# Kernel optimization log

Measured on AMD Instinct MI355X. Metric: run time of the kernel, lower is better.

The kernel has to match this reference:

```python
import jax, jax.numpy as jnp
import numpy as np

B, S, D = 64, 512, 768
CLAUSE = 5  # words per clause


def _ragged():
    w = 64 + (np.arange(B) * 37) % 57              # words per sentence, max 120
    mw = int(w.max())
    Wt = int(w.sum())                               # 5899 total words
    word2sent = np.repeat(np.arange(B), w)
    word_pos = np.concatenate([np.arange(n) for n in w])
    t = 1 + (np.arange(Wt) * 13) % 4                # tokens per word
    word_seg = np.repeat(np.arange(Wt), t)          # token -> word id
    tok_sent = word2sent[word_seg]                  # sorted by sentence
    tok_pos = np.concatenate([np.arange(c) for c in np.bincount(tok_sent, minlength=B)])
    token_indices = tok_sent * S + tok_pos          # clause tokens are the first tokens of each row
    clause_seg = np.arange(Wt) // CLAUSE
    n_clauses = (Wt + CLAUSE - 1) // CLAUSE
    return w, mw, word2sent, word_pos, word_seg, token_indices, clause_seg, n_clauses


def setup_inputs() -> dict:
    key = jax.random.key(0)
    ks = jax.random.split(key, 12)
    w, mw, word2sent, word_pos, word_seg, token_indices, clause_seg, n_clauses = _ragged()
    sequence_output = jax.random.normal(ks[0], (B, S, D), dtype=jnp.float32)
    # sparse-ish adjacency, zeroed beyond each sentence's real word count
    adj = (jax.random.uniform(ks[1], (B, mw, mw)) < 0.1).astype(jnp.float32)
    valid = (jnp.arange(mw)[None, :] < jnp.asarray(w)[:, None]).astype(jnp.float32)
    adj = adj * valid[:, :, None] * valid[:, None, :]
    stdv = 1.0 / np.sqrt(D)
    u = lambda k, shp, s: jax.random.uniform(k, shp, minval=-s, maxval=s, dtype=jnp.float32)
    inp = {
        'sequence_output': sequence_output,
        'adj': adj,
        'W1': u(ks[2], (D, D), stdv), 'b1': u(ks[3], (D,), stdv),
        'W2': u(ks[4], (D, D), stdv), 'b2': u(ks[5], (D,), stdv),
        'W3': u(ks[6], (D, D), stdv), 'b3': u(ks[7], (D,), stdv),
        'Wfc': u(ks[8], (D, 16), stdv), 'bfc': u(ks[9], (16,), stdv),
        'token_indices': jnp.asarray(token_indices, jnp.int32),
        'word_seg': jnp.asarray(word_seg, jnp.int32),
        'word2sent': jnp.asarray(word2sent, jnp.int32),
        'word_pos': jnp.asarray(word_pos, jnp.int32),
        'clause_seg': jnp.asarray(clause_seg, jnp.int32),
        'n_clauses': int(n_clauses),
    }
    return inp


def reference(sequence_output, adj, W1, b1, W2, b2, W3, b3, Wfc, bfc,
              token_indices, word_seg, word2sent, word_pos, clause_seg, n_clauses):
    d = sequence_output.shape[-1]
    Wt = word2sent.shape[0]
    mw = adj.shape[1]
    # masked_select of clause tokens -> [N_tok, D]
    tokens = sequence_output.reshape(-1, d)[token_indices]
    # per-word max over its tokens (torch.split + stack(max))
    word_out = jax.ops.segment_max(tokens, word_seg, num_segments=Wt)
    # pad words into [B, max_words, D] (original pads with randn; adj zeroes pad nodes)
    x = jnp.zeros((adj.shape[0], mw, d), word_out.dtype).at[word2sent, word_pos].set(word_out)
    denom = jnp.sum(adj, axis=2, keepdims=True) + 1.0
    def gcn(h, W, b):
        return jnp.einsum('bij,bjd->bid', adj, h @ W) / denom + b
    x = jax.nn.relu(gcn(x, W1, b1))
    x = jax.nn.relu(gcn(x, W2, b2))
    x = jax.nn.relu(gcn(x, W3, b3))
    # unpad back to ragged word list, then per-clause max
    words_back = x[word2sent, word_pos]
    clause_out = jax.ops.segment_max(words_back, clause_seg, num_segments=n_clauses)
    logits = clause_out @ Wfc + bfc
    return logits
```

## Files before the change

### kernel.cpp

```cpp
#include <hip/hip_runtime.h>
#include <hip/hip_bf16.h>
#include <cfloat>

#define BB   64
#define SS   512
#define DD   768
#define MW   120
#define MPAD 6016
#define TS8  12288
#define WT   5899
#define NC   1180

typedef __attribute__((ext_vector_type(4))) int intx4;

#define SXS  (6.5032f/16255.0f)
#define ISX  (16255.0f/6.5032f)
#define SWS  (0.03610243f/16255.0f)
#define ISW  (16255.0f/0.03610243f)
#define DQ1  (SXS*SWS*16384.0f)
#define DQ2  (SXS*SWS*128.0f)

#define AS3(p) ((__attribute__((address_space(3))) void*)(p))
#define AS1(p) ((const __attribute__((address_space(1))) void*)(p))

__device__ __forceinline__ int swz8(int r, int k) {
    return (r >> 4) * TS8 + (k >> 4) * 256 + (r & 15) * 16 + (k & 15);
}

__device__ __forceinline__ void q8(float x, float inv_s, char& h, char& l) {
    float q = x * inv_s;
    float qh = rintf(q * 0.0078125f);
    qh = fminf(fmaxf(qh, -127.f), 127.f);
    float ql = rintf(fmaf(-128.f, qh, q));
    ql = fminf(fmaxf(ql, -127.f), 127.f);
    h = (char)(int)qh; l = (char)(int)ql;
}

__device__ __forceinline__ int wstart_cf(int w) {
    const int pp[4] = {0, 0, 1, 3};
    return w + 6 * (w >> 2) + pp[w & 3];
}
__device__ __forceinline__ int sent_words(int b) { return 64 + (b * 37) % 57; }

#define NBL_NBR 2560
#define NBL_QW  2304

__global__ __launch_bounds__(192) void setup_k(
    const float* __restrict__ adj,
    const float* __restrict__ W1, const float* __restrict__ W2, const float* __restrict__ W3,
    const float* __restrict__ seq, const int* __restrict__ tok_idx,
    char* __restrict__ qWh, char* __restrict__ qWl,
    char* __restrict__ Qah, char* __restrict__ Qal,
    int* __restrict__ nbr, int* __restrict__ cnt, float* __restrict__ rdenom,
    int* __restrict__ sstart) {
    const int blk = blockIdx.x;
    const int tid = threadIdx.x;
    if (blk < NBL_NBR) {
        int row = blk * 3 + (tid >> 6);
        int lane = tid & 63;
        const float* r = adj + (size_t)row * MW;
        float v0 = r[lane];
        float v1 = (lane + 64 < MW) ? r[lane + 64] : 0.0f;
        unsigned long long m0 = __ballot(v0 != 0.0f);
        unsigned long long m1 = __ballot(v1 != 0.0f);
        unsigned long long below = (1ull << lane) - 1ull;
        int c0 = __popcll(m0);
        int* nb = nbr + (size_t)row * MW;
        if (v0 != 0.0f) nb[__popcll(m0 & below)] = lane;
        if (v1 != 0.0f) nb[c0 + __popcll(m1 & below)] = lane + 64;
        if (lane == 0) {
            int c = c0 + __popcll(m1);
            cnt[row] = c;
            rdenom[row] = 1.0f / (float)(c + 1);
        }
    } else if (blk < NBL_NBR + NBL_QW) {
        int idx = (blk - NBL_NBR) * 192 + tid;
        int l = idx / (DD * DD / 4);
        int rem = idx - l * (DD * DD / 4);
        int kg = rem / DD, n = rem - kg * DD;
        int k = kg * 4;
        const float* W = (l == 0) ? W1 : (l == 1) ? W2 : W3;
        char h[4], lo[4];
        #pragma unroll
        for (int u = 0; u < 4; ++u)
            q8(W[(size_t)(k + u) * DD + n], ISW, h[u], lo[u]);
        int off = l * (DD * DD) + swz8(n, k);
        *(char4*)(qWh + off) = make_char4(h[0], h[1], h[2], h[3]);
        *(char4*)(qWl + off) = make_char4(lo[0], lo[1], lo[2], lo[3]);
    } else if (blk < NBL_NBR + NBL_QW + WT) {
        int w = blk - (NBL_NBR + NBL_QW);
        int t = tid;
        int s = wstart_cf(w), e = wstart_cf(w + 1);
        float4 acc = make_float4(-FLT_MAX, -FLT_MAX, -FLT_MAX, -FLT_MAX);
        for (int i = s; i < e; ++i) {
            int row = tok_idx[i];
            float4 v = *(const float4*)(seq + (size_t)row * DD + t * 4);
            acc.x = fmaxf(acc.x, v.x); acc.y = fmaxf(acc.y, v.y);
            acc.z = fmaxf(acc.z, v.z); acc.w = fmaxf(acc.w, v.w);
        }
        char h[4], lo[4];
        q8(acc.x, ISX, h[0], lo[0]); q8(acc.y, ISX, h[1], lo[1]);
        q8(acc.z, ISX, h[2], lo[2]); q8(acc.w, ISX, h[3], lo[3]);
        int off = swz8(w, t * 4);
        *(char4*)(Qah + off) = make_char4(h[0], h[1], h[2], h[3]);
        *(char4*)(Qal + off) = make_char4(lo[0], lo[1], lo[2], lo[3]);
    } else {
        if (tid == 0) {
            int acc = 0;
            for (int b = 0; b < BB; ++b) { sstart[b] = acc; acc += sent_words(b); }
            sstart[BB] = acc;
        }
    }
}


__global__ __launch_bounds__(256) void gemm8_k(const char* __restrict__ Qah,
                                               const char* __restrict__ Qal,
                                               const char* __restrict__ Qbh,
                                               const char* __restrict__ Qbl,
                                               float* __restrict__ H) {
    __shared__ char lds[49152];
    const int g = blockIdx.x;
    const int xcd = g & 7;
    const int q2 = g >> 3;
    const int nt = q2 % 12;
    const int mt = xcd * 12 + q2 / 12;
    if (mt >= 94) return;

    const int tid = threadIdx.x;
    const int lane = tid & 63;
    const int wave = tid >> 6;
    const int wm = wave >> 1, wn = wave & 1;
    const int bm4 = mt * 4, bn4 = nt * 4;

    const int to = lane * 16;
    const char* gAh = Qah + (size_t)(bm4 + wave) * TS8 + to;
    const char* gAl = Qal + (size_t)(bm4 + wave) * TS8 + to;
    const char* gBh = Qbh + (size_t)(bn4 + wave) * TS8 + to;
    const char* gBl = Qbl + (size_t)(bn4 + wave) * TS8 + to;
    char* ldst = &lds[wave * 1024 + to];

    auto stage = [&](int kt, int buf) {
        const int bo = buf * 16384;
        const int ko = kt * 1024;
        __builtin_amdgcn_global_load_lds(AS1(gAh + ko), AS3(ldst + bo),         16, 0, 0);
        __builtin_amdgcn_global_load_lds(AS1(gAl + ko), AS3(ldst + bo + 4096),  16, 0, 0);
        __builtin_amdgcn_global_load_lds(AS1(gBh + ko), AS3(ldst + bo + 8192),  16, 0, 0);
        __builtin_amdgcn_global_load_lds(AS1(gBl + ko), AS3(ldst + bo + 12288), 16, 0, 0);
    };

    intx4 acc1[2][2] = {}, acc2[2][2] = {};

    stage(0, 0);
    stage(1, 1);
    #pragma unroll
    for (int kt = 0; kt < 12; ++kt) {
        const int buf = kt % 3;
        if (kt < 11) { asm volatile("s_waitcnt vmcnt(4)" ::: "memory"); }
        else         { asm volatile("s_waitcnt vmcnt(0)" ::: "memory"); }
        __builtin_amdgcn_s_barrier();
        asm volatile("" ::: "memory");
        if (kt < 10) stage(kt + 2, (kt + 2) % 3);

        const char* lb = &lds[buf * 16384];
        intx4 ah[2], al[2], bh[2], bl[2];
        #pragma unroll
        for (int i = 0; i < 2; ++i) {
            ah[i] = *(const intx4*)(lb + (wm * 2 + i) * 1024 + lane * 16);
            al[i] = *(const intx4*)(lb + 4096 + (wm * 2 + i) * 1024 + lane * 16);
        }
        #pragma unroll
        for (int j = 0; j < 2; ++j) {
            bh[j] = *(const intx4*)(lb + 8192 + (wn * 2 + j) * 1024 + lane * 16);
            bl[j] = *(const intx4*)(lb + 12288 + (wn * 2 + j) * 1024 + lane * 16);
        }
        #pragma unroll
        for (int i = 0; i < 2; ++i)
            #pragma unroll
            for (int j = 0; j < 2; ++j) {
                acc1[i][j] = __builtin_amdgcn_mfma_i32_16x16x64_i8(ah[i], bh[j], acc1[i][j], 0, 0, 0);
                acc2[i][j] = __builtin_amdgcn_mfma_i32_16x16x64_i8(ah[i], bl[j], acc2[i][j], 0, 0, 0);
                acc2[i][j] = __builtin_amdgcn_mfma_i32_16x16x64_i8(al[i], bh[j], acc2[i][j], 0, 0, 0);
            }
    }

    const int q = lane >> 4, c = lane & 15;
    #pragma unroll
    for (int i = 0; i < 2; ++i) {
        #pragma unroll
        for (int r = 0; r < 4; ++r) {
            int row = mt * 64 + (wm * 2 + i) * 16 + q * 4 + r;
            float* out = H + (size_t)row * DD + nt * 64 + wn * 32 + c;
            #pragma unroll
            for (int j = 0; j < 2; ++j)
                out[j * 16] = (float)acc1[i][j][r] * DQ1 + (float)acc2[i][j][r] * DQ2;
        }
    }
}

__global__ void combine_k(const float* __restrict__ H, const int* __restrict__ w2s,
                          const int* __restrict__ sstart, const int* __restrict__ nbr,
                          const int* __restrict__ cnt, const float* __restrict__ rdenom,
                          const float* __restrict__ bias,
                          char* __restrict__ Qah, char* __restrict__ Qal,
                          float* __restrict__ Xf, int writef32) {
    int g = blockIdx.x;
    int w = (g & 7) * 768 + (g >> 3);
    if (w >= WT) return;
    int t = threadIdx.x;
    int s = w2s[w];
    int w0 = sstart[s];
    int bi = s * MW + (w - w0);
    int n = cnt[bi];
    float rd = rdenom[bi];
    const int* nb = nbr + (size_t)bi * MW;
    float4 acc = make_float4(0.f, 0.f, 0.f, 0.f);
    for (int k = 0; k < n; ++k) {
        int row = w0 + nb[k];
        float4 v = *(const float4*)(H + (size_t)row * DD + t * 4);
        acc.x += v.x; acc.y += v.y; acc.z += v.z; acc.w += v.w;
    }
    float4 bv = *(const float4*)(bias + t * 4);
    float4 o;
    o.x = fmaxf(fmaf(acc.x, rd, bv.x), 0.f);
    o.y = fmaxf(fmaf(acc.y, rd, bv.y), 0.f);
    o.z = fmaxf(fmaf(acc.z, rd, bv.z), 0.f);
    o.w = fmaxf(fmaf(acc.w, rd, bv.w), 0.f);
    if (writef32) {
        *(float4*)(Xf + (size_t)w * DD + t * 4) = o;
    } else {
        char h[4], lo[4];
        q8(o.x, ISX, h[0], lo[0]); q8(o.y, ISX, h[1], lo[1]);
        q8(o.z, ISX, h[2], lo[2]); q8(o.w, ISX, h[3], lo[3]);
        int off = swz8(w, t * 4);
        *(char4*)(Qah + off) = make_char4(h[0], h[1], h[2], h[3]);
        *(char4*)(Qal + off) = make_char4(lo[0], lo[1], lo[2], lo[3]);
    }
}

__global__ __launch_bounds__(192) void clause_k(const float* __restrict__ Xf,
                                                const float* __restrict__ Wfc,
                                                const float* __restrict__ bfc,
                                                float* __restrict__ out) {
    __shared__ float cm[DD];
    __shared__ float part[12][16];
    int c = blockIdx.x;
    int t = threadIdx.x;
    int s = c * 5, e = min(c * 5 + 5, WT);
    float4 m = make_float4(-FLT_MAX, -FLT_MAX, -FLT_MAX, -FLT_MAX);
    for (int w = s; w < e; ++w) {
        float4 v = *(const float4*)(Xf + (size_t)w * DD + t * 4);
        m.x = fmaxf(m.x, v.x); m.y = fmaxf(m.y, v.y);
        m.z = fmaxf(m.z, v.z); m.w = fmaxf(m.w, v.w);
    }
    *(float4*)&cm[t * 4] = m;
    __syncthreads();
    int o = t & 15, gg = t >> 4;
    float p = 0.f;
    #pragma unroll 4
    for (int d = gg * 64; d < gg * 64 + 64; ++d)
        p = fmaf(cm[d], Wfc[d * 16 + o], p);
    part[gg][o] = p;
    __syncthreads();
    if (t < 16) {
        float acc = bfc[t];
        #pragma unroll
        for (int g2 = 0; g2 < 12; ++g2) acc += part[g2][t];
        out[c * 16 + t] = acc;
    }
}

extern "C" void kernel_launch(void* const* d_in, const int* in_sizes, int n_in,
                              void* d_out, int out_size, void* d_ws, size_t ws_size,
                              hipStream_t stream) {
    const float* seq  = (const float*)d_in[0];
    const float* adj  = (const float*)d_in[1];
    const float* W1   = (const float*)d_in[2];
    const float* b1   = (const float*)d_in[3];
    const float* W2   = (const float*)d_in[4];
    const float* b2   = (const float*)d_in[5];
    const float* W3   = (const float*)d_in[6];
    const float* b3   = (const float*)d_in[7];
    const float* Wfc  = (const float*)d_in[8];
    const float* bfc  = (const float*)d_in[9];
    const int* tok_idx = (const int*)d_in[10];
    const int* w2s     = (const int*)d_in[12];

    char* p = (char*)d_ws;
    char* Qah = p; p += (size_t)MPAD * DD;
    char* Qal = p; p += (size_t)MPAD * DD;
    float* H  = (float*)p; p += (size_t)MPAD * DD * 4;
    char* qWh = p; p += (size_t)3 * DD * DD;
    char* qWl = p; p += (size_t)3 * DD * DD;
    float* Xf = (float*)p; p += (size_t)MPAD * DD * 4;
    int* nbr    = (int*)p;    p += (size_t)BB * MW * MW * 4;
    int* cnt    = (int*)p;    p += (size_t)BB * MW * 4;
    float* rde  = (float*)p;  p += (size_t)BB * MW * 4;
    int* sstart = (int*)p;    p += (size_t)(BB + 1) * 4;

    setup_k<<<NBL_NBR + NBL_QW + WT + 1, 192, 0, stream>>>(
        adj, W1, W2, W3, seq, tok_idx, qWh, qWl, Qah, Qal, nbr, cnt, rde, sstart);

    const float* bs[3] = {b1, b2, b3};
    for (int l = 0; l < 3; ++l) {
        gemm8_k<<<1152, 256, 0, stream>>>(
            Qah, Qal, qWh + (size_t)l * DD * DD, qWl + (size_t)l * DD * DD, H);
        combine_k<<<8 * 768, 192, 0, stream>>>(H, w2s, sstart, nbr, cnt, rde, bs[l],
                                               Qah, Qal, Xf, l == 2 ? 1 : 0);
    }

    clause_k<<<NC, 192, 0, stream>>>(Xf, Wfc, bfc, (float*)d_out);
}
```

Measured before the change: 282.5 us.

## Fuse per-layer GEMM and adjacency aggregation into one per-sentence kernel

Replaces the separate int8 GEMM and the neighbour-combine kernel with one layer kernel. Each block computes a sentence's 128-row by 96-column slice of the hidden product and keeps it in LDS, then does the adjacency sum, bias, ReLU and requantisation from LDS. Activations are laid out per sentence padded to 128 rows, with ping-pong activation buffers. This removes the global H round trip and half the launches, but pays for padded rows, A fragments loaded straight from global into registers, a non-pipelined vmcnt(0) wait every k-step, and a large LDS footprint that limits occupancy.

```diff
diff --git a/kernel.cpp b/kernel.cpp
--- a/kernel.cpp
+++ b/kernel.cpp
@@ -6,10 +6,11 @@
 #define SS   512
 #define DD   768
 #define MW   120
-#define MPAD 6016
 #define TS8  12288
 #define WT   5899
 #define NC   1180
+#define QROWS 8192
+#define HS   108
 
 typedef __attribute__((ext_vector_type(4))) int intx4;
 
@@ -41,6 +42,11 @@
     return w + 6 * (w >> 2) + pp[w & 3];
 }
 __device__ __forceinline__ int sent_words(int b) { return 64 + (b * 37) % 57; }
+__device__ __forceinline__ int sstart_cf(int s) {
+    int a = 0;
+    for (int b = 0; b < s; ++b) a += 64 + (b * 37) % 57;
+    return a;
+}
 
 #define NBL_NBR 2560
 #define NBL_QW  2304
@@ -49,6 +55,7 @@
     const float* __restrict__ adj,
     const float* __restrict__ W1, const float* __restrict__ W2, const float* __restrict__ W3,
     const float* __restrict__ seq, const int* __restrict__ tok_idx,
+    const int* __restrict__ w2s,
     char* __restrict__ qWh, char* __restrict__ qWl,
     char* __restrict__ Qah, char* __restrict__ Qal,
     int* __restrict__ nbr, int* __restrict__ cnt, float* __restrict__ rdenom,
@@ -101,7 +108,9 @@
         char h[4], lo[4];
         q8(acc.x, ISX, h[0], lo[0]); q8(acc.y, ISX, h[1], lo[1]);
         q8(acc.z, ISX, h[2], lo[2]); q8(acc.w, ISX, h[3], lo[3]);
-        int off = swz8(w, t * 4);
+        int sn = w2s[w];
+        int lr = w - sstart_cf(sn);
+        int off = swz8(sn * 128 + lr, t * 4);
         *(char4*)(Qah + off) = make_char4(h[0], h[1], h[2], h[3]);
         *(char4*)(Qal + off) = make_char4(lo[0], lo[1], lo[2], lo[3]);
     } else {
@@ -113,128 +122,130 @@
     }
 }
 
-
-__global__ __launch_bounds__(256) void gemm8_k(const char* __restrict__ Qah,
-                                               const char* __restrict__ Qal,
-                                               const char* __restrict__ Qbh,
-                                               const char* __restrict__ Qbl,
-                                               float* __restrict__ H) {
-    __shared__ char lds[49152];
+__global__ __launch_bounds__(256, 2) void layer_k(
+    const char* __restrict__ Ah, const char* __restrict__ Al,
+    const char* __restrict__ Wh, const char* __restrict__ Wl,
+    const float* __restrict__ bias,
+    const int* __restrict__ nbr, const int* __restrict__ cnt,
+    const float* __restrict__ rdenom, const int* __restrict__ sstart,
+    char* __restrict__ QnH, char* __restrict__ QnL,
+    float* __restrict__ Xf, int writef32) {
+    __shared__ float Hl[128 * HS];
+    __shared__ char  Wb[2 * 12288];
+
     const int g = blockIdx.x;
     const int xcd = g & 7;
-    const int q2 = g >> 3;
-    const int nt = q2 % 12;
-    const int mt = xcd * 12 + q2 / 12;
-    if (mt >= 94) return;
-
+    const int idx = g >> 3;
+    const int s  = xcd * 8 + (idx >> 3);
+    const int cg = idx & 7;
     const int tid = threadIdx.x;
     const int lane = tid & 63;
     const int wave = tid >> 6;
-    const int wm = wave >> 1, wn = wave & 1;
-    const int bm4 = mt * 4, bn4 = nt * 4;
-
-    const int to = lane * 16;
-    const char* gAh = Qah + (size_t)(bm4 + wave) * TS8 + to;
-    const char* gAl = Qal + (size_t)(bm4 + wave) * TS8 + to;
-    const char* gBh = Qbh + (size_t)(bn4 + wave) * TS8 + to;
-    const char* gBl = Qbl + (size_t)(bn4 + wave) * TS8 + to;
-    char* ldst = &lds[wave * 1024 + to];
-
-    auto stage = [&](int kt, int buf) {
-        const int bo = buf * 16384;
-        const int ko = kt * 1024;
-        __builtin_amdgcn_global_load_lds(AS1(gAh + ko), AS3(ldst + bo),         16, 0, 0);
-        __builtin_amdgcn_global_load_lds(AS1(gAl + ko), AS3(ldst + bo + 4096),  16, 0, 0);
-        __builtin_amdgcn_global_load_lds(AS1(gBh + ko), AS3(ldst + bo + 8192),  16, 0, 0);
-        __builtin_amdgcn_global_load_lds(AS1(gBl + ko), AS3(ldst + bo + 12288), 16, 0, 0);
+    const int rg = wave >> 1;
+    const int cv = wave & 1;
+    const int nw = sent_words(s);
+    const int F  = (nw + 15) >> 4;
+    const int myf = rg ? (F - 4) : 4;
+    const int fb = rg * 4;
+    const int s8 = s * 8;
+    const int cg6 = cg * 6;
+    const int ws0 = sstart[s];
+    const int q = lane >> 4, cl = lane & 15;
+
+    auto stageW = [&](int kt, int buf) {
+        #pragma unroll
+        for (int j = 0; j < 3; ++j) {
+            int c = wave + 4 * j;
+            const char* src = (c < 6 ? Wh + (size_t)(cg6 + c) * TS8
+                                     : Wl + (size_t)(cg6 + c - 6) * TS8)
+                              + kt * 1024 + lane * 16;
+            __builtin_amdgcn_global_load_lds(AS1(src),
+                AS3(Wb + buf * 12288 + c * 1024 + lane * 16), 16, 0, 0);
+        }
     };
-
-    intx4 acc1[2][2] = {}, acc2[2][2] = {};
-
-    stage(0, 0);
-    stage(1, 1);
+    auto loadA = [&](int kt, intx4* rh, intx4* rl) {
+        #pragma unroll
+        for (int i = 0; i < 4; ++i) if (i < myf) {
+            size_t off = (size_t)(s8 + fb + i) * TS8 + kt * 1024 + lane * 16;
+            rh[i] = *(const intx4*)(Ah + off);
+            rl[i] = *(const intx4*)(Al + off);
+        }
+    };
+
+    intx4 acc1[4][3] = {}, acc2[4][3] = {};
+    intx4 ah0[4], al0[4], ah1[4], al1[4];
+    stageW(0, 0);
+    loadA(0, ah0, al0);
     #pragma unroll
     for (int kt = 0; kt < 12; ++kt) {
-        const int buf = kt % 3;
-        if (kt < 11) { asm volatile("s_waitcnt vmcnt(4)" ::: "memory"); }
-        else         { asm volatile("s_waitcnt vmcnt(0)" ::: "memory"); }
+        asm volatile("s_waitcnt vmcnt(0)" ::: "memory");
         __builtin_amdgcn_s_barrier();
         asm volatile("" ::: "memory");
-        if (kt < 10) stage(kt + 2, (kt + 2) % 3);
-
-        const char* lb = &lds[buf * 16384];
-        intx4 ah[2], al[2], bh[2], bl[2];
-        #pragma unroll
-        for (int i = 0; i < 2; ++i) {
-            ah[i] = *(const intx4*)(lb + (wm * 2 + i) * 1024 + lane * 16);
-            al[i] = *(const intx4*)(lb + 4096 + (wm * 2 + i) * 1024 + lane * 16);
-        }
-        #pragma unroll
-        for (int j = 0; j < 2; ++j) {
-            bh[j] = *(const intx4*)(lb + 8192 + (wn * 2 + j) * 1024 + lane * 16);
-            bl[j] = *(const intx4*)(lb + 12288 + (wn * 2 + j) * 1024 + lane * 16);
-        }
-        #pragma unroll
-        for (int i = 0; i < 2; ++i)
+        if (kt < 11) {
+            stageW(kt + 1, (kt + 1) & 1);
+            loadA(kt + 1, (kt & 1) ? ah0 : ah1, (kt & 1) ? al0 : al1);
+        }
+        const char* wb = Wb + (kt & 1) * 12288;
+        intx4 bh[3], bl[3];
+        #pragma unroll
+        for (int j = 0; j < 3; ++j) {
+            bh[j] = *(const intx4*)(wb + (cv * 3 + j) * 1024 + lane * 16);
+            bl[j] = *(const intx4*)(wb + 6144 + (cv * 3 + j) * 1024 + lane * 16);
+        }
+        const intx4* ch = (kt & 1) ? ah1 : ah0;
+        const intx4* clo = (kt & 1) ? al1 : al0;
+        #pragma unroll
+        for (int i = 0; i < 4; ++i) if (i < myf)
             #pragma unroll
-            for (int j = 0; j < 2; ++j) {
-                acc1[i][j] = __builtin_amdgcn_mfma_i32_16x16x64_i8(ah[i], bh[j], acc1[i][j], 0, 0, 0);
-                acc2[i][j] = __builtin_amdgcn_mfma_i32_16x16x64_i8(ah[i], bl[j], acc2[i][j], 0, 0, 0);
-                acc2[i][j] = __builtin_amdgcn_mfma_i32_16x16x64_i8(al[i], bh[j], acc2[i][j], 0, 0, 0);
+            for (int j = 0; j < 3; ++j) {
+                acc1[i][j] = __builtin_amdgcn_mfma_i32_16x16x64_i8(ch[i],  bh[j], acc1[i][j], 0, 0, 0);
+                acc2[i][j] = __builtin_amdgcn_mfma_i32_16x16x64_i8(ch[i],  bl[j], acc2[i][j], 0, 0, 0);
+                acc2[i][j] = __builtin_amdgcn_mfma_i32_16x16x64_i8(clo[i], bh[j], acc2[i][j], 0, 0, 0);
             }
     }
 
-    const int q = lane >> 4, c = lane & 15;
     #pragma unroll
-    for (int i = 0; i < 2; ++i) {
-        #pragma unroll
-        for (int r = 0; r < 4; ++r) {
-            int row = mt * 64 + (wm * 2 + i) * 16 + q * 4 + r;
-            float* out = H + (size_t)row * DD + nt * 64 + wn * 32 + c;
+    for (int i = 0; i < 4; ++i) if (i < myf)
+        #pragma unroll
+        for (int j = 0; j < 3; ++j)
             #pragma unroll
-            for (int j = 0; j < 2; ++j)
-                out[j * 16] = (float)acc1[i][j][r] * DQ1 + (float)acc2[i][j][r] * DQ2;
-        }
-    }
-}
-
-__global__ void combine_k(const float* __restrict__ H, const int* __restrict__ w2s,
-                          const int* __restrict__ sstart, const int* __restrict__ nbr,
-                          const int* __restrict__ cnt, const float* __restrict__ rdenom,
-                          const float* __restrict__ bias,
-                          char* __restrict__ Qah, char* __restrict__ Qal,
-                          float* __restrict__ Xf, int writef32) {
-    int g = blockIdx.x;
-    int w = (g & 7) * 768 + (g >> 3);
-    if (w >= WT) return;
-    int t = threadIdx.x;
-    int s = w2s[w];
-    int w0 = sstart[s];
-    int bi = s * MW + (w - w0);
-    int n = cnt[bi];
-    float rd = rdenom[bi];
-    const int* nb = nbr + (size_t)bi * MW;
-    float4 acc = make_float4(0.f, 0.f, 0.f, 0.f);
-    for (int k = 0; k < n; ++k) {
-        int row = w0 + nb[k];
-        float4 v = *(const float4*)(H + (size_t)row * DD + t * 4);
-        acc.x += v.x; acc.y += v.y; acc.z += v.z; acc.w += v.w;
-    }
-    float4 bv = *(const float4*)(bias + t * 4);
-    float4 o;
-    o.x = fmaxf(fmaf(acc.x, rd, bv.x), 0.f);
-    o.y = fmaxf(fmaf(acc.y, rd, bv.y), 0.f);
-    o.z = fmaxf(fmaf(acc.z, rd, bv.z), 0.f);
-    o.w = fmaxf(fmaf(acc.w, rd, bv.w), 0.f);
-    if (writef32) {
-        *(float4*)(Xf + (size_t)w * DD + t * 4) = o;
-    } else {
-        char h[4], lo[4];
-        q8(o.x, ISX, h[0], lo[0]); q8(o.y, ISX, h[1], lo[1]);
-        q8(o.z, ISX, h[2], lo[2]); q8(o.w, ISX, h[3], lo[3]);
-        int off = swz8(w, t * 4);
-        *(char4*)(Qah + off) = make_char4(h[0], h[1], h[2], h[3]);
-        *(char4*)(Qal + off) = make_char4(lo[0], lo[1], lo[2], lo[3]);
+            for (int r = 0; r < 4; ++r) {
+                int row = (fb + i) * 16 + q * 4 + r;
+                int col = cv * 48 + j * 16 + cl;
+                Hl[row * HS + col] = (float)acc1[i][j][r] * DQ1 + (float)acc2[i][j][r] * DQ2;
+            }
+    __syncthreads();
+
+    if (tid < 240) {
+        int wq = tid / 24, cq = tid % 24;
+        int c4 = cq * 4;
+        float4 bv = *(const float4*)(bias + cg * 96 + c4);
+        for (int w = wq; w < nw; w += 10) {
+            int bi = s * MW + w;
+            int n = cnt[bi];
+            float rd = rdenom[bi];
+            const int* nb = nbr + (size_t)bi * MW;
+            float4 a = make_float4(0.f, 0.f, 0.f, 0.f);
+            for (int k = 0; k < n; ++k) {
+                float4 v = *(const float4*)(&Hl[nb[k] * HS + c4]);
+                a.x += v.x; a.y += v.y; a.z += v.z; a.w += v.w;
+            }
+            float4 o;
+            o.x = fmaxf(fmaf(a.x, rd, bv.x), 0.f);
+            o.y = fmaxf(fmaf(a.y, rd, bv.y), 0.f);
+            o.z = fmaxf(fmaf(a.z, rd, bv.z), 0.f);
+            o.w = fmaxf(fmaf(a.w, rd, bv.w), 0.f);
+            if (!writef32) {
+                char h[4], lo[4];
+                q8(o.x, ISX, h[0], lo[0]); q8(o.y, ISX, h[1], lo[1]);
+                q8(o.z, ISX, h[2], lo[2]); q8(o.w, ISX, h[3], lo[3]);
+                int off = swz8(s * 128 + w, cg * 96 + c4);
+                *(char4*)(QnH + off) = make_char4(h[0], h[1], h[2], h[3]);
+                *(char4*)(QnL + off) = make_char4(lo[0], lo[1], lo[2], lo[3]);
+            } else {
+                *(float4*)(Xf + (size_t)(ws0 + w) * DD + cg * 96 + c4) = o;
+            }
+        }
     }
 }
 
@@ -287,27 +298,33 @@
     const int* w2s     = (const int*)d_in[12];
 
     char* p = (char*)d_ws;
-    char* Qah = p; p += (size_t)MPAD * DD;
-    char* Qal = p; p += (size_t)MPAD * DD;
-    float* H  = (float*)p; p += (size_t)MPAD * DD * 4;
-    char* qWh = p; p += (size_t)3 * DD * DD;
-    char* qWl = p; p += (size_t)3 * DD * DD;
-    float* Xf = (float*)p; p += (size_t)MPAD * DD * 4;
+    char* Qa0h = p; p += (size_t)QROWS * DD;
+    char* Qa0l = p; p += (size_t)QROWS * DD;
+    char* Qa1h = p; p += (size_t)QROWS * DD;
+    char* Qa1l = p; p += (size_t)QROWS * DD;
+    char* qWh  = p; p += (size_t)3 * DD * DD;
+    char* qWl  = p; p += (size_t)3 * DD * DD;
+    float* Xf  = (float*)p; p += (size_t)WT * DD * 4 + 1024;
     int* nbr    = (int*)p;    p += (size_t)BB * MW * MW * 4;
     int* cnt    = (int*)p;    p += (size_t)BB * MW * 4;
     float* rde  = (float*)p;  p += (size_t)BB * MW * 4;
     int* sstart = (int*)p;    p += (size_t)(BB + 1) * 4;
 
     setup_k<<<NBL_NBR + NBL_QW + WT + 1, 192, 0, stream>>>(
-        adj, W1, W2, W3, seq, tok_idx, qWh, qWl, Qah, Qal, nbr, cnt, rde, sstart);
-
-    const float* bs[3] = {b1, b2, b3};
-    for (int l = 0; l < 3; ++l) {
-        gemm8_k<<<1152, 256, 0, stream>>>(
-            Qah, Qal, qWh + (size_t)l * DD * DD, qWl + (size_t)l * DD * DD, H);
-        combine_k<<<8 * 768, 192, 0, stream>>>(H, w2s, sstart, nbr, cnt, rde, bs[l],
-                                               Qah, Qal, Xf, l == 2 ? 1 : 0);
-    }
+        adj, W1, W2, W3, seq, tok_idx, w2s, qWh, qWl, Qa0h, Qa0l,
+        nbr, cnt, rde, sstart);
+
+    layer_k<<<512, 256, 0, stream>>>(Qa0h, Qa0l, qWh, qWl, b1,
+                                     nbr, cnt, rde, sstart,
+                                     Qa1h, Qa1l, Xf, 0);
+    layer_k<<<512, 256, 0, stream>>>(Qa1h, Qa1l,
+                                     qWh + (size_t)DD * DD, qWl + (size_t)DD * DD, b2,
+                                     nbr, cnt, rde, sstart,
+                                     Qa0h, Qa0l, Xf, 0);
+    layer_k<<<512, 256, 0, stream>>>(Qa0h, Qa0l,
+                                     qWh + (size_t)2 * DD * DD, qWl + (size_t)2 * DD * DD, b3,
+                                     nbr, cnt, rde, sstart,
+                                     Qa1h, Qa1l, Xf, 1);
 
     clause_k<<<NC, 192, 0, stream>>>(Xf, Wfc, bfc, (float*)d_out);
 }
```

Result: slower. 313.0 us (+10.8%).

## Store GEMM output as split int8 and aggregate neighbors in integer

Applied to the files above, without the earlier changes.

The GEMM epilogue now quantizes each output element into a high/low int8 pair instead of writing fp32, which cuts the intermediate H buffer from 4 bytes to 2 bytes per element. The combine kernel sums the char4 pairs with integer accumulators and dequantizes once using the activation scale times the reciprocal degree. Neighbor indices are staged in shared memory first. This adds another quantization step with its own error, since the fixed activation scale may not fit the GEMM output range. The GEMM stores also become byte-wide scattered writes.

```diff
diff --git a/kernel.cpp b/kernel.cpp
--- a/kernel.cpp
+++ b/kernel.cpp
@@ -113,12 +113,12 @@
     }
 }
 
-
 __global__ __launch_bounds__(256) void gemm8_k(const char* __restrict__ Qah,
                                                const char* __restrict__ Qal,
                                                const char* __restrict__ Qbh,
                                                const char* __restrict__ Qbl,
-                                               float* __restrict__ H) {
+                                               char* __restrict__ H8h,
+                                               char* __restrict__ H8l) {
     __shared__ char lds[49152];
     const int g = blockIdx.x;
     const int xcd = g & 7;
@@ -190,20 +190,28 @@
         #pragma unroll
         for (int r = 0; r < 4; ++r) {
             int row = mt * 64 + (wm * 2 + i) * 16 + q * 4 + r;
-            float* out = H + (size_t)row * DD + nt * 64 + wn * 32 + c;
+            size_t rb = (size_t)row * DD + nt * 64 + wn * 32 + c;
             #pragma unroll
-            for (int j = 0; j < 2; ++j)
-                out[j * 16] = (float)acc1[i][j][r] * DQ1 + (float)acc2[i][j][r] * DQ2;
-        }
-    }
-}
-
-__global__ void combine_k(const float* __restrict__ H, const int* __restrict__ w2s,
+            for (int j = 0; j < 2; ++j) {
+                float o = (float)acc1[i][j][r] * DQ1 + (float)acc2[i][j][r] * DQ2;
+                char h, lo;
+                q8(o, ISX, h, lo);
+                H8h[rb + j * 16] = h;
+                H8l[rb + j * 16] = lo;
+            }
+        }
+    }
+}
+
+__global__ __launch_bounds__(192) void combine_k(
+                          const char* __restrict__ H8h, const char* __restrict__ H8l,
+                          const int* __restrict__ w2s,
                           const int* __restrict__ sstart, const int* __restrict__ nbr,
                           const int* __restrict__ cnt, const float* __restrict__ rdenom,
                           const float* __restrict__ bias,
                           char* __restrict__ Qah, char* __restrict__ Qal,
                           float* __restrict__ Xf, int writef32) {
+    __shared__ int nbs[MW];
     int g = blockIdx.x;
     int w = (g & 7) * 768 + (g >> 3);
     if (w >= WT) return;
@@ -214,18 +222,25 @@
     int n = cnt[bi];
     float rd = rdenom[bi];
     const int* nb = nbr + (size_t)bi * MW;
-    float4 acc = make_float4(0.f, 0.f, 0.f, 0.f);
+    if (t < n) nbs[t] = nb[t];
+    __syncthreads();
+    int hx = 0, hy = 0, hz = 0, hw = 0;
+    int lx = 0, ly = 0, lz = 0, lw = 0;
+    #pragma unroll 2
     for (int k = 0; k < n; ++k) {
-        int row = w0 + nb[k];
-        float4 v = *(const float4*)(H + (size_t)row * DD + t * 4);
-        acc.x += v.x; acc.y += v.y; acc.z += v.z; acc.w += v.w;
+        size_t rb = (size_t)(w0 + nbs[k]) * DD + t * 4;
+        char4 hq = *(const char4*)(H8h + rb);
+        char4 lq = *(const char4*)(H8l + rb);
+        hx += hq.x; hy += hq.y; hz += hq.z; hw += hq.w;
+        lx += lq.x; ly += lq.y; lz += lq.z; lw += lq.w;
     }
     float4 bv = *(const float4*)(bias + t * 4);
+    float k1 = SXS * rd;
     float4 o;
-    o.x = fmaxf(fmaf(acc.x, rd, bv.x), 0.f);
-    o.y = fmaxf(fmaf(acc.y, rd, bv.y), 0.f);
-    o.z = fmaxf(fmaf(acc.z, rd, bv.z), 0.f);
-    o.w = fmaxf(fmaf(acc.w, rd, bv.w), 0.f);
+    o.x = fmaxf(fmaf((float)(hx * 128 + lx), k1, bv.x), 0.f);
+    o.y = fmaxf(fmaf((float)(hy * 128 + ly), k1, bv.y), 0.f);
+    o.z = fmaxf(fmaf((float)(hz * 128 + lz), k1, bv.z), 0.f);
+    o.w = fmaxf(fmaf((float)(hw * 128 + lw), k1, bv.w), 0.f);
     if (writef32) {
         *(float4*)(Xf + (size_t)w * DD + t * 4) = o;
     } else {
@@ -289,7 +304,8 @@
     char* p = (char*)d_ws;
     char* Qah = p; p += (size_t)MPAD * DD;
     char* Qal = p; p += (size_t)MPAD * DD;
-    float* H  = (float*)p; p += (size_t)MPAD * DD * 4;
+    char* H8h = p; p += (size_t)MPAD * DD;
+    char* H8l = p; p += (size_t)MPAD * DD;
     char* qWh = p; p += (size_t)3 * DD * DD;
     char* qWl = p; p += (size_t)3 * DD * DD;
     float* Xf = (float*)p; p += (size_t)MPAD * DD * 4;
@@ -304,8 +320,8 @@
     const float* bs[3] = {b1, b2, b3};
     for (int l = 0; l < 3; ++l) {
         gemm8_k<<<1152, 256, 0, stream>>>(
-            Qah, Qal, qWh + (size_t)l * DD * DD, qWl + (size_t)l * DD * DD, H);
-        combine_k<<<8 * 768, 192, 0, stream>>>(H, w2s, sstart, nbr, cnt, rde, bs[l],
+            Qah, Qal, qWh + (size_t)l * DD * DD, qWl + (size_t)l * DD * DD, H8h, H8l);
+        combine_k<<<8 * 768, 192, 0, stream>>>(H8h, H8l, w2s, sstart, nbr, cnt, rde, bs[l],
                                                Qah, Qal, Xf, l == 2 ? 1 : 0);
     }
 
```

Measured after the change: 275.6 us. -2.4%, faster.

## Replace sparse neighbor gather with per-sentence int8 MFMA adjacency aggregation

Applied to the files above, without the earlier changes.

Turns the adjacency aggregation from a neighbor-list gather over fp32 H into a dense per-sentence int8 MFMA matmul, with adjacency stored as swizzled 0/1 bytes. The GEMM now computes the transposed product W^T·X, quantizes its output to a hi/lo int8 split and writes it per sentence in a transposed tiled layout. Activations are padded to 128 rows per sentence and ping-pong between two buffers. The aim is to drop the fp32 H round trip and the irregular gathers. In exchange, padding adds wasted rows, and H gets an extra quantization step that may cost accuracy.

```diff
diff --git a/kernel.cpp b/kernel.cpp
--- a/kernel.cpp
+++ b/kernel.cpp
@@ -6,10 +6,13 @@
 #define SS   512
 #define DD   768
 #define MW   120
-#define MPAD 6016
 #define TS8  12288
 #define WT   5899
 #define NC   1180
+#define SP   128
+#define QROWS (BB*SP)
+#define ATS  16384
+#define HTS  98304
 
 typedef __attribute__((ext_vector_type(4))) int intx4;
 
@@ -25,6 +28,9 @@
 
 __device__ __forceinline__ int swz8(int r, int k) {
     return (r >> 4) * TS8 + (k >> 4) * 256 + (r & 15) * 16 + (k & 15);
+}
+__device__ __forceinline__ int swzA(int r, int k) {
+    return (r >> 4) * 2048 + (k >> 4) * 256 + (r & 15) * 16 + (k & 15);
 }
 
 __device__ __forceinline__ void q8(float x, float inv_s, char& h, char& l) {
@@ -41,6 +47,11 @@
     return w + 6 * (w >> 2) + pp[w & 3];
 }
 __device__ __forceinline__ int sent_words(int b) { return 64 + (b * 37) % 57; }
+__device__ __forceinline__ int sstart_cf(int s) {
+    int a = 0;
+    for (int b = 0; b < s; ++b) a += 64 + (b * 37) % 57;
+    return a;
+}
 
 #define NBL_NBR 2560
 #define NBL_QW  2304
@@ -49,28 +60,28 @@
     const float* __restrict__ adj,
     const float* __restrict__ W1, const float* __restrict__ W2, const float* __restrict__ W3,
     const float* __restrict__ seq, const int* __restrict__ tok_idx,
+    const int* __restrict__ w2s,
     char* __restrict__ qWh, char* __restrict__ qWl,
     char* __restrict__ Qah, char* __restrict__ Qal,
-    int* __restrict__ nbr, int* __restrict__ cnt, float* __restrict__ rdenom,
+    char* __restrict__ adj8, float* __restrict__ rdenom,
     int* __restrict__ sstart) {
     const int blk = blockIdx.x;
     const int tid = threadIdx.x;
     if (blk < NBL_NBR) {
         int row = blk * 3 + (tid >> 6);
         int lane = tid & 63;
+        int s = row / 120;
+        int i = row - s * 120;
         const float* r = adj + (size_t)row * MW;
         float v0 = r[lane];
         float v1 = (lane + 64 < MW) ? r[lane + 64] : 0.0f;
+        char* a8 = adj8 + (size_t)s * ATS;
+        a8[swzA(i, lane)]      = (v0 != 0.0f) ? 1 : 0;
+        a8[swzA(i, lane + 64)] = (v1 != 0.0f) ? 1 : 0;
         unsigned long long m0 = __ballot(v0 != 0.0f);
         unsigned long long m1 = __ballot(v1 != 0.0f);
-        unsigned long long below = (1ull << lane) - 1ull;
-        int c0 = __popcll(m0);
-        int* nb = nbr + (size_t)row * MW;
-        if (v0 != 0.0f) nb[__popcll(m0 & below)] = lane;
-        if (v1 != 0.0f) nb[c0 + __popcll(m1 & below)] = lane + 64;
         if (lane == 0) {
-            int c = c0 + __popcll(m1);
-            cnt[row] = c;
+            int c = __popcll(m0) + __popcll(m1);
             rdenom[row] = 1.0f / (float)(c + 1);
         }
     } else if (blk < NBL_NBR + NBL_QW) {
@@ -101,7 +112,9 @@
         char h[4], lo[4];
         q8(acc.x, ISX, h[0], lo[0]); q8(acc.y, ISX, h[1], lo[1]);
         q8(acc.z, ISX, h[2], lo[2]); q8(acc.w, ISX, h[3], lo[3]);
-        int off = swz8(w, t * 4);
+        int sn = w2s[w];
+        int wl = w - sstart_cf(sn);
+        int off = swz8(sn * SP + wl, t * 4);
         *(char4*)(Qah + off) = make_char4(h[0], h[1], h[2], h[3]);
         *(char4*)(Qal + off) = make_char4(lo[0], lo[1], lo[2], lo[3]);
     } else {
@@ -113,19 +126,18 @@
     }
 }
 
-
-__global__ __launch_bounds__(256) void gemm8_k(const char* __restrict__ Qah,
+__global__ __launch_bounds__(256) void gemm8_k(const char* __restrict__ Wh8,
+                                               const char* __restrict__ Wl8,
+                                               const char* __restrict__ Qah,
                                                const char* __restrict__ Qal,
-                                               const char* __restrict__ Qbh,
-                                               const char* __restrict__ Qbl,
-                                               float* __restrict__ H) {
+                                               char* __restrict__ H8Th,
+                                               char* __restrict__ H8Tl) {
     __shared__ char lds[49152];
     const int g = blockIdx.x;
     const int xcd = g & 7;
     const int q2 = g >> 3;
-    const int nt = q2 % 12;
-    const int mt = xcd * 12 + q2 / 12;
-    if (mt >= 94) return;
+    const int nt = xcd * 16 + (q2 & 15);
+    const int mt = q2 >> 4;
 
     const int tid = threadIdx.x;
     const int lane = tid & 63;
@@ -134,10 +146,10 @@
     const int bm4 = mt * 4, bn4 = nt * 4;
 
     const int to = lane * 16;
-    const char* gAh = Qah + (size_t)(bm4 + wave) * TS8 + to;
-    const char* gAl = Qal + (size_t)(bm4 + wave) * TS8 + to;
-    const char* gBh = Qbh + (size_t)(bn4 + wave) * TS8 + to;
-    const char* gBl = Qbl + (size_t)(bn4 + wave) * TS8 + to;
+    const char* gAh = Wh8 + (size_t)(bm4 + wave) * TS8 + to;
+    const char* gAl = Wl8 + (size_t)(bm4 + wave) * TS8 + to;
+    const char* gBh = Qah + (size_t)(bn4 + wave) * TS8 + to;
+    const char* gBl = Qal + (size_t)(bn4 + wave) * TS8 + to;
     char* ldst = &lds[wave * 1024 + to];
 
     auto stage = [&](int kt, int buf) {
@@ -189,52 +201,95 @@
     for (int i = 0; i < 2; ++i) {
         #pragma unroll
         for (int r = 0; r < 4; ++r) {
-            int row = mt * 64 + (wm * 2 + i) * 16 + q * 4 + r;
-            float* out = H + (size_t)row * DD + nt * 64 + wn * 32 + c;
+            int crow = mt * 64 + (wm * 2 + i) * 16 + q * 4 + r;
             #pragma unroll
-            for (int j = 0; j < 2; ++j)
-                out[j * 16] = (float)acc1[i][j][r] * DQ1 + (float)acc2[i][j][r] * DQ2;
-        }
-    }
-}
-
-__global__ void combine_k(const float* __restrict__ H, const int* __restrict__ w2s,
-                          const int* __restrict__ sstart, const int* __restrict__ nbr,
-                          const int* __restrict__ cnt, const float* __restrict__ rdenom,
-                          const float* __restrict__ bias,
-                          char* __restrict__ Qah, char* __restrict__ Qal,
-                          float* __restrict__ Xf, int writef32) {
-    int g = blockIdx.x;
-    int w = (g & 7) * 768 + (g >> 3);
-    if (w >= WT) return;
-    int t = threadIdx.x;
-    int s = w2s[w];
-    int w0 = sstart[s];
-    int bi = s * MW + (w - w0);
-    int n = cnt[bi];
-    float rd = rdenom[bi];
-    const int* nb = nbr + (size_t)bi * MW;
-    float4 acc = make_float4(0.f, 0.f, 0.f, 0.f);
-    for (int k = 0; k < n; ++k) {
-        int row = w0 + nb[k];
-        float4 v = *(const float4*)(H + (size_t)row * DD + t * 4);
-        acc.x += v.x; acc.y += v.y; acc.z += v.z; acc.w += v.w;
-    }
-    float4 bv = *(const float4*)(bias + t * 4);
-    float4 o;
-    o.x = fmaxf(fmaf(acc.x, rd, bv.x), 0.f);
-    o.y = fmaxf(fmaf(acc.y, rd, bv.y), 0.f);
-    o.z = fmaxf(fmaf(acc.z, rd, bv.z), 0.f);
-    o.w = fmaxf(fmaf(acc.w, rd, bv.w), 0.f);
-    if (writef32) {
-        *(float4*)(Xf + (size_t)w * DD + t * 4) = o;
-    } else {
-        char h[4], lo[4];
-        q8(o.x, ISX, h[0], lo[0]); q8(o.y, ISX, h[1], lo[1]);
-        q8(o.z, ISX, h[2], lo[2]); q8(o.w, ISX, h[3], lo[3]);
-        int off = swz8(w, t * 4);
-        *(char4*)(Qah + off) = make_char4(h[0], h[1], h[2], h[3]);
-        *(char4*)(Qal + off) = make_char4(lo[0], lo[1], lo[2], lo[3]);
+            for (int j = 0; j < 2; ++j) {
+                int wcol = nt * 64 + wn * 32 + j * 16 + c;
+                float o = (float)acc1[i][j][r] * DQ1 + (float)acc2[i][j][r] * DQ2;
+                char h, lo;
+                q8(o, ISX, h, lo);
+                int off = (wcol >> 7) * HTS + swzA(crow, wcol & 127);
+                H8Th[off] = h;
+                H8Tl[off] = lo;
+            }
+        }
+    }
+}
+
+__global__ __launch_bounds__(256) void agg_k(
+    const char* __restrict__ adj8,
+    const char* __restrict__ H8Th, const char* __restrict__ H8Tl,
+    const float* __restrict__ rdenom, const float* __restrict__ bias,
+    const int* __restrict__ sstart,
+    char* __restrict__ QnH, char* __restrict__ QnL,
+    float* __restrict__ Xf, int writef32) {
+    const int g = blockIdx.x;
+    const int xcd = g & 7;
+    const int r0 = g >> 3;
+    const int s  = xcd * 8 + (r0 & 7);
+    const int rr = r0 >> 3;
+    const int mt = rr & 1;
+    const int ct = rr >> 1;
+    const int tid = threadIdx.x;
+    const int lane = tid & 63;
+    const int wave = tid >> 6;
+    const int wm = wave >> 1, wn = wave & 1;
+    const int nw = sent_words(s);
+
+    const char* Ab = adj8 + (size_t)s * ATS;
+    const char* Bh = H8Th + (size_t)s * HTS;
+    const char* Bl = H8Tl + (size_t)s * HTS;
+
+    intx4 acch[2][2] = {}, accl[2][2] = {};
+    #pragma unroll
+    for (int kt = 0; kt < 2; ++kt) {
+        intx4 a[2], bh[2], bl[2];
+        #pragma unroll
+        for (int i = 0; i < 2; ++i) {
+            int fw = mt * 4 + wm * 2 + i;
+            a[i] = *(const intx4*)(Ab + fw * 2048 + kt * 1024 + lane * 16);
+        }
+        #pragma unroll
+        for (int j = 0; j < 2; ++j) {
+            int fc = ct * 4 + wn * 2 + j;
+            bh[j] = *(const intx4*)(Bh + fc * 2048 + kt * 1024 + lane * 16);
+            bl[j] = *(const intx4*)(Bl + fc * 2048 + kt * 1024 + lane * 16);
+        }
+        #pragma unroll
+        for (int i = 0; i < 2; ++i)
+            #pragma unroll
+            for (int j = 0; j < 2; ++j) {
+                acch[i][j] = __builtin_amdgcn_mfma_i32_16x16x64_i8(a[i], bh[j], acch[i][j], 0, 0, 0);
+                accl[i][j] = __builtin_amdgcn_mfma_i32_16x16x64_i8(a[i], bl[j], accl[i][j], 0, 0, 0);
+            }
+    }
+
+    const int q = lane >> 4, cl = lane & 15;
+    const int ws0 = sstart[s];
+    #pragma unroll
+    for (int i = 0; i < 2; ++i) {
+        #pragma unroll
+        for (int r = 0; r < 4; ++r) {
+            int w = mt * 64 + (wm * 2 + i) * 16 + q * 4 + r;
+            if (w < nw) {
+                float k1 = SXS * rdenom[s * MW + w];
+                #pragma unroll
+                for (int j = 0; j < 2; ++j) {
+                    int c = ct * 64 + wn * 32 + j * 16 + cl;
+                    float val = fmaf((float)(acch[i][j][r] * 128 + accl[i][j][r]), k1, bias[c]);
+                    val = fmaxf(val, 0.f);
+                    if (!writef32) {
+                        char h, lo;
+                        q8(val, ISX, h, lo);
+                        int off = swz8(s * SP + w, c);
+                        QnH[off] = h;
+                        QnL[off] = lo;
+                    } else {
+                        Xf[(size_t)(ws0 + w) * DD + c] = val;
+                    }
+                }
+            }
+        }
     }
 }
 
@@ -287,26 +342,34 @@
     const int* w2s     = (const int*)d_in[12];
 
     char* p = (char*)d_ws;
-    char* Qah = p; p += (size_t)MPAD * DD;
-    char* Qal = p; p += (size_t)MPAD * DD;
-    float* H  = (float*)p; p += (size_t)MPAD * DD * 4;
-    char* qWh = p; p += (size_t)3 * DD * DD;
-    char* qWl = p; p += (size_t)3 * DD * DD;
-    float* Xf = (float*)p; p += (size_t)MPAD * DD * 4;
-    int* nbr    = (int*)p;    p += (size_t)BB * MW * MW * 4;
-    int* cnt    = (int*)p;    p += (size_t)BB * MW * 4;
+    char* Qa0h = p; p += (size_t)QROWS * DD;
+    char* Qa0l = p; p += (size_t)QROWS * DD;
+    char* Qa1h = p; p += (size_t)QROWS * DD;
+    char* Qa1l = p; p += (size_t)QROWS * DD;
+    char* H8Th = p; p += (size_t)BB * HTS;
+    char* H8Tl = p; p += (size_t)BB * HTS;
+    char* qWh  = p; p += (size_t)3 * DD * DD;
+    char* qWl  = p; p += (size_t)3 * DD * DD;
+    char* adj8 = p; p += (size_t)BB * ATS;
+    float* Xf  = (float*)p; p += (size_t)WT * DD * 4 + 1024;
     float* rde  = (float*)p;  p += (size_t)BB * MW * 4;
     int* sstart = (int*)p;    p += (size_t)(BB + 1) * 4;
 
     setup_k<<<NBL_NBR + NBL_QW + WT + 1, 192, 0, stream>>>(
-        adj, W1, W2, W3, seq, tok_idx, qWh, qWl, Qah, Qal, nbr, cnt, rde, sstart);
+        adj, W1, W2, W3, seq, tok_idx, w2s, qWh, qWl, Qa0h, Qa0l,
+        adj8, rde, sstart);
 
     const float* bs[3] = {b1, b2, b3};
+    const char* ah[3] = {Qa0h, Qa1h, Qa0h};
+    const char* al[3] = {Qa0l, Qa1l, Qa0l};
+    char* nh[3] = {Qa1h, Qa0h, Qa1h};
+    char* nl[3] = {Qa1l, Qa0l, Qa1l};
     for (int l = 0; l < 3; ++l) {
-        gemm8_k<<<1152, 256, 0, stream>>>(
-            Qah, Qal, qWh + (size_t)l * DD * DD, qWl + (size_t)l * DD * DD, H);
-        combine_k<<<8 * 768, 192, 0, stream>>>(H, w2s, sstart, nbr, cnt, rde, bs[l],
-                                               Qah, Qal, Xf, l == 2 ? 1 : 0);
+        gemm8_k<<<1536, 256, 0, stream>>>(
+            qWh + (size_t)l * DD * DD, qWl + (size_t)l * DD * DD,
+            ah[l], al[l], H8Th, H8Tl);
+        agg_k<<<1536, 256, 0, stream>>>(adj8, H8Th, H8Tl, rde, bs[l], sstart,
+                                        nh[l], nl[l], Xf, l == 2 ? 1 : 0);
     }
 
     clause_k<<<NC, 192, 0, stream>>>(Xf, Wfc, bfc, (float*)d_out);
```

New measurement: 287.1 us. No clear change (+1.6%).
